# Kernel optimization log

Measured on AMD Instinct MI355X. Metric: run time of the kernel, lower is better.

Reference implementation:

```python
import jax, jax.numpy as jnp
import numpy as np

NUM_HEADS = 16

def setup_inputs() -> dict:
    key = jax.random.key(0)
    ks = jax.random.split(key, 5)
    B, T, C = 2, 2048, 1024
    s = 0.02
    return {
        "x": jax.random.normal(ks[0], (B, T, C), dtype=jnp.float32),
        "attn_w": jax.random.normal(ks[1], (3 * C, C), dtype=jnp.float32) * s,
        "attn_b": jax.random.normal(ks[2], (3 * C,), dtype=jnp.float32) * s,
        "proj_w": jax.random.normal(ks[3], (C, C), dtype=jnp.float32) * s,
        "proj_b": jax.random.normal(ks[4], (C,), dtype=jnp.float32) * s,
    }

def reference(x, attn_w, attn_b, proj_w, proj_b):
    B, T, C = x.shape
    H = NUM_HEADS
    D = C // H
    # fused QKV projection (torch Linear: x @ W^T + b)
    qkv = x @ attn_w.T + attn_b                      # [B, T, 3C]
    q, k, v = jnp.split(qkv, 3, axis=-1)             # each [B, T, C]
    # split heads -> [B, H, T, D]
    def heads(t):
        return t.reshape(B, T, H, D).transpose(0, 2, 1, 3)
    q, k, v = heads(q), heads(k), heads(v)
    scale = 1.0 / jnp.sqrt(jnp.asarray(D, dtype=x.dtype))
    scores = jnp.einsum("bhtd,bhsd->bhts", q, k) * scale   # [B, H, T, T]
    causal = jnp.tril(jnp.ones((T, T), dtype=bool))
    scores = jnp.where(causal[None, None], scores, jnp.asarray(-jnp.inf, dtype=scores.dtype))
    att = jax.nn.softmax(scores, axis=-1)
    out = jnp.einsum("bhts,bhsd->bhtd", att, v)      # [B, H, T, D]
    out = out.transpose(0, 2, 1, 3).reshape(B, T, C)
    return out @ proj_w.T + proj_b
```

## Files before the change

### kernel.cpp

```cpp
#include <hip/hip_runtime.h>
#include <hip/hip_bf16.h>

typedef __bf16 bf16_t;
typedef __bf16 bf16x4 __attribute__((ext_vector_type(4)));
typedef __bf16 bf16x8 __attribute__((ext_vector_type(8)));
typedef float f32x4 __attribute__((ext_vector_type(4)));
typedef float f32x8 __attribute__((ext_vector_type(8)));

#define MFMA16(a, b, c) __builtin_amdgcn_mfma_f32_16x16x32_bf16(a, b, c, 0, 0, 0)

#define GLOAD_LDS16(g, l)                                              \
  __builtin_amdgcn_global_load_lds(                                    \
      (const __attribute__((address_space(1))) unsigned int*)(g),      \
      (__attribute__((address_space(3))) unsigned int*)(l), 16, 0, 0)

constexpr int B = 2, T = 2048, C = 1024, H = 16, D = 64;
constexpr int NQKV = 3 * C;
constexpr int M = B * T;

__global__ __launch_bounds__(256) void cvt_kernel(
    const float* __restrict__ s0, bf16_t* __restrict__ d0, int n0,
    const float* __restrict__ s1, bf16_t* __restrict__ d1, int n1,
    const float* __restrict__ s2, bf16_t* __restrict__ d2, int n2)
{
  const float* s; bf16_t* d; int n;
  if (blockIdx.y == 0)      { s = s0; d = d0; n = n0; }
  else if (blockIdx.y == 1) { s = s1; d = d1; n = n1; }
  else                      { s = s2; d = d2; n = n2; }
  const int idx = (blockIdx.x * 256 + threadIdx.x) * 8;
  if (idx >= n) return;
  f32x8 t = *(const f32x8*)(s + idx);
  bf16x8 r;
#pragma unroll
  for (int j = 0; j < 8; ++j) r[j] = (bf16_t)t[j];
  *(bf16x8*)(d + idx) = r;
}

__device__ __forceinline__ void gemm_mainloop(
    const bf16_t* __restrict__ A, const bf16_t* __restrict__ Wt,
    int K, int m0, int n0, bf16_t* ldsA, bf16_t* ldsB, f32x4 acc[4][4])
{
  const int tid  = threadIdx.x;
  const int wv   = tid >> 6;
  const int lane = tid & 63;
  const int col  = lane & 15;
  const int quad = lane >> 4;
  const int lrow = lane >> 3;
  const int cpos = lane & 7;
  const int wm = wv >> 1, wn = wv & 1;

  const bf16_t* ag[4]; const bf16_t* bg[4];
#pragma unroll
  for (int j = 0; j < 4; ++j) {
    const int row = wv * 32 + j * 8 + lrow;
    const int sc  = cpos ^ lrow;
    ag[j] = A  + (size_t)(m0 + row) * K + sc * 8;
    bg[j] = Wt + (size_t)(n0 + row) * K + sc * 8;
  }

  const int xa = quad ^ (col & 7);

  for (int kt = 0; kt < K; kt += 64) {
#pragma unroll
    for (int j = 0; j < 4; ++j) {
      GLOAD_LDS16(ag[j], ldsA + (wv * 32 + j * 8) * 64);
      GLOAD_LDS16(bg[j], ldsB + (wv * 32 + j * 8) * 64);
      ag[j] += 64; bg[j] += 64;
    }
    __syncthreads();
#pragma unroll
    for (int ks = 0; ks < 2; ++ks) {
      const int xk = (xa ^ (ks * 4)) * 8;
      bf16x8 af[4], bfr[4];
#pragma unroll
      for (int mi = 0; mi < 4; ++mi)
        af[mi] = *(const bf16x8*)(ldsA + (wm * 64 + mi * 16 + col) * 64 + xk);
#pragma unroll
      for (int ni = 0; ni < 4; ++ni)
        bfr[ni] = *(const bf16x8*)(ldsB + (wn * 64 + ni * 16 + col) * 64 + xk);
#pragma unroll
      for (int mi = 0; mi < 4; ++mi)
#pragma unroll
        for (int ni = 0; ni < 4; ++ni)
          acc[mi][ni] = MFMA16(af[mi], bfr[ni], acc[mi][ni]);
    }
    __syncthreads();
  }
}

__global__ __launch_bounds__(256) void qkv_gemm_kernel(
    const bf16_t* __restrict__ x, const bf16_t* __restrict__ w,
    const float* __restrict__ bias,
    bf16_t* __restrict__ qws, bf16_t* __restrict__ kws, bf16_t* __restrict__ vws)
{
  __shared__ __align__(16) bf16_t ldsA[128 * 64];
  __shared__ __align__(16) bf16_t ldsB[128 * 64];
  const int lane = threadIdx.x & 63;
  const int wv   = threadIdx.x >> 6;
  const int col  = lane & 15;
  const int quad = lane >> 4;
  const int wm = wv >> 1, wn = wv & 1;
  const int m0 = blockIdx.y * 128;
  const int n0 = blockIdx.x * 128;

  f32x4 acc[4][4] = {};
  gemm_mainloop(x, w, C, m0, n0, ldsA, ldsB, acc);

#pragma unroll
  for (int ni = 0; ni < 4; ++ni) {
    const int n = n0 + wn * 64 + ni * 16 + col;
    const float bval = bias[n];
    const int which = n >> 10;
    const int c = n & (C - 1);
    const int h = c >> 6;
    const int d = c & 63;
#pragma unroll
    for (int mi = 0; mi < 4; ++mi) {
#pragma unroll
      for (int r = 0; r < 4; ++r) {
        const int m = m0 + wm * 64 + mi * 16 + quad * 4 + r;
        const int b = m >> 11;
        const int t = m & (T - 1);
        const bf16_t bv = (bf16_t)(acc[mi][ni][r] + bval);
        const size_t bh = (size_t)(b * H + h);
        if (which == 0)      qws[(bh * T + t) * D + d] = bv;
        else if (which == 1) kws[(bh * T + t) * D + d] = bv;
        else {
          const int tp = (t & ~63) | ((t & 15) << 2) | ((t >> 4) & 3);
          vws[(bh * D + d) * T + tp] = bv;
        }
      }
    }
  }
}

__global__ __launch_bounds__(256) void attn_kernel(
    const bf16_t* __restrict__ qws, const bf16_t* __restrict__ kws,
    const bf16_t* __restrict__ vws, bf16_t* __restrict__ yws)
{
  const int bh = blockIdx.y;
  const int tid  = threadIdx.x;
  const int wv   = tid >> 6;
  const int lane = tid & 63;
  const int col  = lane & 15;
  const int quad = lane >> 4;

  const bf16_t* Q  = qws + (size_t)bh * T * D;
  const bf16_t* K  = kws + (size_t)bh * T * D;
  const bf16_t* Vt = vws + (size_t)bh * D * T;

  __shared__ __align__(16) bf16_t ldsK[2][64 * 64];
  __shared__ __align__(16) bf16_t ldsV[2][64 * 64];
  __shared__ __align__(16) bf16_t ldsP[4][16 * 64];
  bf16_t* ldsPw = ldsP[wv];

  const float cscale = 0.125f * 1.44269504088896340736f;

  const int xs   = col & 7;
  const int cxq  = (quad ^ xs) * 8;
  const int lr8  = lane >> 3;
  const int ksrc = (lane & 7) ^ lr8;
  const int pxor = (quad & 1) * 4;
  const int b = bh >> 4;
  const int h = bh & 15;

#pragma unroll
  for (int half = 0; half < 2; ++half) {
    const int qt = half == 0 ? (31 - (int)blockIdx.x) : (int)blockIdx.x;
    const int t0 = qt * 64;
    const int tw = t0 + 16 * wv;
    const int niter = qt + 1;

    bf16x8 qf0 = *(const bf16x8*)(Q + (size_t)(tw + col) * D + quad * 8);
    bf16x8 qf1 = *(const bf16x8*)(Q + (size_t)(tw + col) * D + 32 + quad * 8);

    f32x4 o[4] = {};
    f32x4 lp = {};

    __syncthreads();

#pragma unroll
    for (int j = 0; j < 2; ++j) {
      GLOAD_LDS16(K + (size_t)(16 * wv + j * 8 + lr8) * D + ksrc * 8,
                  ldsK[0] + (16 * wv + j * 8) * 64);
      GLOAD_LDS16(Vt + (size_t)(16 * wv + j * 8 + lr8) * T + ksrc * 8,
                  ldsV[0] + (16 * wv + j * 8) * 64);
    }

    for (int it = 0; it < niter; ++it) {
      const int s0 = it * 64;
      __syncthreads();

      if (it + 1 < niter) {
        const int sn = s0 + 64;
        bf16_t* dK = ldsK[(it + 1) & 1];
        bf16_t* dV = ldsV[(it + 1) & 1];
#pragma unroll
        for (int j = 0; j < 2; ++j) {
          GLOAD_LDS16(K + (size_t)(sn + 16 * wv + j * 8 + lr8) * D + ksrc * 8,
                      dK + (16 * wv + j * 8) * 64);
          GLOAD_LDS16(Vt + (size_t)(16 * wv + j * 8 + lr8) * T + sn + ksrc * 8,
                      dV + (16 * wv + j * 8) * 64);
        }
      }

      const bf16_t* bK = ldsK[it & 1];
      const bf16_t* bV = ldsV[it & 1];

      f32x4 sc[4];
#pragma unroll
      for (int kb = 0; kb < 4; ++kb) {
        const bf16_t* kr = bK + (kb * 16 + col) * 64;
        bf16x8 kf0 = *(const bf16x8*)(kr + cxq);
        bf16x8 kf1 = *(const bf16x8*)(kr + (cxq ^ 32));
        f32x4 a = {};
        a = MFMA16(qf0, kf0, a);
        a = MFMA16(qf1, kf1, a);
        sc[kb] = a;
      }

      const bool diag = (s0 == t0);
#pragma unroll
      for (int r = 0; r < 4; ++r) {
        const int prow = (quad * 4 + r) * 64;
        const int pxr  = pxor + r;
        bf16x4 pw;
#pragma unroll
        for (int kb = 0; kb < 4; ++kb) {
          float p = __builtin_amdgcn_exp2f(sc[kb][r] * cscale);
          if (diag && (s0 + kb * 16 + col > tw + quad * 4 + r)) p = 0.0f;
          lp[r] += p;
          pw[kb] = (bf16_t)p;
        }
        *(bf16x4*)(ldsPw + prow + (((col >> 1) ^ pxr) * 8) + (col & 1) * 4) = pw;
      }

#pragma unroll
      for (int ks = 0; ks < 2; ++ks) {
        const int xk = cxq ^ (ks * 32);
        bf16x8 pa = *(const bf16x8*)(ldsPw + col * 64 + xk);
#pragma unroll
        for (int ni = 0; ni < 4; ++ni) {
          bf16x8 vf = *(const bf16x8*)(bV + (ni * 16 + col) * 64 + xk);
          o[ni] = MFMA16(pa, vf, o[ni]);
        }
      }
    }

#pragma unroll
    for (int r = 0; r < 4; ++r) {
      float l = lp[r];
#pragma unroll
      for (int off = 1; off < 16; off <<= 1)
        l += __shfl_xor(l, off);
      const float rl = 1.0f / l;
      const int t = tw + quad * 4 + r;
#pragma unroll
      for (int ni = 0; ni < 4; ++ni) {
        const int d = ni * 16 + col;
        yws[((size_t)(b * T + t)) * C + h * D + d] = (bf16_t)(o[ni][r] * rl);
      }
    }
  }
}

__global__ __launch_bounds__(256) void proj_gemm_kernel(
    const bf16_t* __restrict__ y, const bf16_t* __restrict__ w,
    const float* __restrict__ bias, float* __restrict__ out)
{
  __shared__ __align__(16) bf16_t ldsA[128 * 64];
  __shared__ __align__(16) bf16_t ldsB[128 * 64];
  const int lane = threadIdx.x & 63;
  const int wv   = threadIdx.x >> 6;
  const int col  = lane & 15;
  const int quad = lane >> 4;
  const int wm = wv >> 1, wn = wv & 1;
  const int m0 = blockIdx.y * 128;
  const int n0 = blockIdx.x * 128;

  f32x4 acc[4][4] = {};
  gemm_mainloop(y, w, C, m0, n0, ldsA, ldsB, acc);

#pragma unroll
  for (int ni = 0; ni < 4; ++ni) {
    const int n = n0 + wn * 64 + ni * 16 + col;
    const float bval = bias[n];
#pragma unroll
    for (int mi = 0; mi < 4; ++mi) {
#pragma unroll
      for (int r = 0; r < 4; ++r) {
        const int m = m0 + wm * 64 + mi * 16 + quad * 4 + r;
        out[(size_t)m * C + n] = acc[mi][ni][r] + bval;
      }
    }
  }
}

extern "C" void kernel_launch(void* const* d_in, const int* in_sizes, int n_in,
                              void* d_out, int out_size, void* d_ws, size_t ws_size,
                              hipStream_t stream) {
  const float* x      = (const float*)d_in[0];
  const float* attn_w = (const float*)d_in[1];
  const float* attn_b = (const float*)d_in[2];
  const float* proj_w = (const float*)d_in[3];
  const float* proj_b = (const float*)d_in[4];
  float* out = (float*)d_out;

  const size_t E = (size_t)B * H * T * D;
  char* ws = (char*)d_ws;
  bf16_t* qws = (bf16_t*)(ws);
  bf16_t* kws = (bf16_t*)(ws + 2 * E);
  bf16_t* vws = (bf16_t*)(ws + 4 * E);
  bf16_t* yws = (bf16_t*)(ws + 6 * E);
  bf16_t* xb  = (bf16_t*)(ws + 8 * E);
  bf16_t* awb = (bf16_t*)(ws + 10 * E);
  bf16_t* pwb = (bf16_t*)(ws + 11 * E + E / 2);

  const int NX = M * C, NAW = NQKV * C, NPW = C * C;
  cvt_kernel<<<dim3(NX / 2048, 3), 256, 0, stream>>>(
      x, xb, NX, attn_w, awb, NAW, proj_w, pwb, NPW);
  qkv_gemm_kernel<<<dim3(NQKV / 128, M / 128), 256, 0, stream>>>(
      xb, awb, attn_b, qws, kws, vws);
  attn_kernel<<<dim3(16, B * H), 256, 0, stream>>>(qws, kws, vws, yws);
  proj_gemm_kernel<<<dim3(C / 128, M / 128), 256, 0, stream>>>(
      yws, pwb, proj_b, out);
}
```

Before: 200.3 us.

## Double-buffer GEMM LDS tiles and shrink projection GEMM N-tile to 64

Rewrites the shared GEMM mainloop to double-buffer the A/B LDS tiles. The next K-slice is issued with global_load_lds while the current one feeds MFMAs, which drops one barrier per iteration. The projection GEMM now uses 128x64 tiles, doubling its block count from 256 to 512 so more of the GPU's CUs are occupied. The cost is doubled LDS per block, which can cut occupancy, and smaller projection tiles give less operand reuse.

```diff
diff --git a/kernel.cpp b/kernel.cpp
--- a/kernel.cpp
+++ b/kernel.cpp
@@ -36,55 +36,73 @@
   *(bf16x8*)(d + idx) = r;
 }
 
-__device__ __forceinline__ void gemm_mainloop(
+template<int BN, int NI>
+__device__ __forceinline__ void gemm_mainloop_db(
     const bf16_t* __restrict__ A, const bf16_t* __restrict__ Wt,
-    int K, int m0, int n0, bf16_t* ldsA, bf16_t* ldsB, f32x4 acc[4][4])
+    const int K, const int m0, const int n0,
+    bf16_t* ldsA0, bf16_t* ldsA1, bf16_t* ldsB0, bf16_t* ldsB1,
+    f32x4 acc[4][NI])
 {
   const int tid  = threadIdx.x;
   const int wv   = tid >> 6;
   const int lane = tid & 63;
   const int col  = lane & 15;
   const int quad = lane >> 4;
-  const int lrow = lane >> 3;
+  const int lr8  = lane >> 3;
   const int cpos = lane & 7;
   const int wm = wv >> 1, wn = wv & 1;
-
-  const bf16_t* ag[4]; const bf16_t* bg[4];
-#pragma unroll
-  for (int j = 0; j < 4; ++j) {
-    const int row = wv * 32 + j * 8 + lrow;
-    const int sc  = cpos ^ lrow;
-    ag[j] = A  + (size_t)(m0 + row) * K + sc * 8;
-    bg[j] = Wt + (size_t)(n0 + row) * K + sc * 8;
-  }
+  constexpr int BJ = BN / 32;
+  constexpr int BRW = BN / 4;
+
+  const bf16_t* ag[4]; const bf16_t* bg[BJ];
+#pragma unroll
+  for (int j = 0; j < 4; ++j)
+    ag[j] = A + (size_t)(m0 + wv * 32 + j * 8 + lr8) * K + (cpos ^ lr8) * 8;
+#pragma unroll
+  for (int j = 0; j < BJ; ++j)
+    bg[j] = Wt + (size_t)(n0 + wv * BRW + j * 8 + lr8) * K + (cpos ^ lr8) * 8;
 
   const int xa = quad ^ (col & 7);
-
-  for (int kt = 0; kt < K; kt += 64) {
-#pragma unroll
-    for (int j = 0; j < 4; ++j) {
-      GLOAD_LDS16(ag[j], ldsA + (wv * 32 + j * 8) * 64);
-      GLOAD_LDS16(bg[j], ldsB + (wv * 32 + j * 8) * 64);
-      ag[j] += 64; bg[j] += 64;
-    }
+  const int niter = K / 64;
+
+#pragma unroll
+  for (int j = 0; j < 4; ++j)
+    GLOAD_LDS16(ag[j], ldsA0 + (wv * 32 + j * 8) * 64);
+#pragma unroll
+  for (int j = 0; j < BJ; ++j)
+    GLOAD_LDS16(bg[j], ldsB0 + (wv * BRW + j * 8) * 64);
+
+  for (int it = 0; it < niter; ++it) {
     __syncthreads();
+    const bf16_t* cA = (it & 1) ? ldsA1 : ldsA0;
+    const bf16_t* cB = (it & 1) ? ldsB1 : ldsB0;
+    if (it + 1 < niter) {
+      bf16_t* nA = (it & 1) ? ldsA0 : ldsA1;
+      bf16_t* nB = (it & 1) ? ldsB0 : ldsB1;
+      const int off = (it + 1) * 64;
+#pragma unroll
+      for (int j = 0; j < 4; ++j)
+        GLOAD_LDS16(ag[j] + off, nA + (wv * 32 + j * 8) * 64);
+#pragma unroll
+      for (int j = 0; j < BJ; ++j)
+        GLOAD_LDS16(bg[j] + off, nB + (wv * BRW + j * 8) * 64);
+    }
 #pragma unroll
     for (int ks = 0; ks < 2; ++ks) {
       const int xk = (xa ^ (ks * 4)) * 8;
-      bf16x8 af[4], bfr[4];
+      bf16x8 af[4], bfr[NI];
 #pragma unroll
       for (int mi = 0; mi < 4; ++mi)
-        af[mi] = *(const bf16x8*)(ldsA + (wm * 64 + mi * 16 + col) * 64 + xk);
-#pragma unroll
-      for (int ni = 0; ni < 4; ++ni)
-        bfr[ni] = *(const bf16x8*)(ldsB + (wn * 64 + ni * 16 + col) * 64 + xk);
+        af[mi] = *(const bf16x8*)(cA + (wm * 64 + mi * 16 + col) * 64 + xk);
+#pragma unroll
+      for (int ni = 0; ni < NI; ++ni)
+        bfr[ni] = *(const bf16x8*)(cB + (wn * (NI * 16) + ni * 16 + col) * 64 + xk);
 #pragma unroll
       for (int mi = 0; mi < 4; ++mi)
 #pragma unroll
-        for (int ni = 0; ni < 4; ++ni)
+        for (int ni = 0; ni < NI; ++ni)
           acc[mi][ni] = MFMA16(af[mi], bfr[ni], acc[mi][ni]);
     }
-    __syncthreads();
   }
 }
 
@@ -93,8 +111,8 @@
     const float* __restrict__ bias,
     bf16_t* __restrict__ qws, bf16_t* __restrict__ kws, bf16_t* __restrict__ vws)
 {
-  __shared__ __align__(16) bf16_t ldsA[128 * 64];
-  __shared__ __align__(16) bf16_t ldsB[128 * 64];
+  __shared__ __align__(16) bf16_t ldsA[2][128 * 64];
+  __shared__ __align__(16) bf16_t ldsB[2][128 * 64];
   const int lane = threadIdx.x & 63;
   const int wv   = threadIdx.x >> 6;
   const int col  = lane & 15;
@@ -104,7 +122,8 @@
   const int n0 = blockIdx.x * 128;
 
   f32x4 acc[4][4] = {};
-  gemm_mainloop(x, w, C, m0, n0, ldsA, ldsB, acc);
+  gemm_mainloop_db<128, 4>(x, w, C, m0, n0,
+                           ldsA[0], ldsA[1], ldsB[0], ldsB[1], acc);
 
 #pragma unroll
   for (int ni = 0; ni < 4; ++ni) {
@@ -268,22 +287,23 @@
     const bf16_t* __restrict__ y, const bf16_t* __restrict__ w,
     const float* __restrict__ bias, float* __restrict__ out)
 {
-  __shared__ __align__(16) bf16_t ldsA[128 * 64];
-  __shared__ __align__(16) bf16_t ldsB[128 * 64];
+  __shared__ __align__(16) bf16_t ldsA[2][128 * 64];
+  __shared__ __align__(16) bf16_t ldsB[2][64 * 64];
   const int lane = threadIdx.x & 63;
   const int wv   = threadIdx.x >> 6;
   const int col  = lane & 15;
   const int quad = lane >> 4;
   const int wm = wv >> 1, wn = wv & 1;
   const int m0 = blockIdx.y * 128;
-  const int n0 = blockIdx.x * 128;
-
-  f32x4 acc[4][4] = {};
-  gemm_mainloop(y, w, C, m0, n0, ldsA, ldsB, acc);
-
-#pragma unroll
-  for (int ni = 0; ni < 4; ++ni) {
-    const int n = n0 + wn * 64 + ni * 16 + col;
+  const int n0 = blockIdx.x * 64;
+
+  f32x4 acc[4][2] = {};
+  gemm_mainloop_db<64, 2>(y, w, C, m0, n0,
+                          ldsA[0], ldsA[1], ldsB[0], ldsB[1], acc);
+
+#pragma unroll
+  for (int ni = 0; ni < 2; ++ni) {
+    const int n = n0 + wn * 32 + ni * 16 + col;
     const float bval = bias[n];
 #pragma unroll
     for (int mi = 0; mi < 4; ++mi) {
@@ -322,6 +342,6 @@
   qkv_gemm_kernel<<<dim3(NQKV / 128, M / 128), 256, 0, stream>>>(
       xb, awb, attn_b, qws, kws, vws);
   attn_kernel<<<dim3(16, B * H), 256, 0, stream>>>(qws, kws, vws, yws);
-  proj_gemm_kernel<<<dim3(C / 128, M / 128), 256, 0, stream>>>(
+  proj_gemm_kernel<<<dim3(C / 64, M / 128), 256, 0, stream>>>(
       yws, pwb, proj_b, out);
 }
```

New measurement: 196.9 us. Within noise of the previous version (-1.7%).
